# Performance work log

Hardware: AMD Instinct MI355X
Metric: run time of the kernel (lower is better)

## Reference

```python
import jax, jax.numpy as jnp
import numpy as np

TOKENS = 8192
MODEL_DIM = 4096
PROMPT_DIM = 64
NUM_EXPERTS = 8
TOP_K = 2
EPS = float(np.finfo(np.float32).eps)


def setup_inputs() -> dict:
    key = jax.random.key(0)
    k1, k2, k3 = jax.random.split(key, 3)
    x = jax.random.normal(k1, (TOKENS, MODEL_DIM), dtype=jnp.float32)
    prompt = jax.random.normal(k2, (TOKENS, PROMPT_DIM), dtype=jnp.float32)
    # gate linear: Linear(model_dim + prompt_dim, num_experts, bias=True)
    W = jax.random.normal(k3, (MODEL_DIM + PROMPT_DIM, NUM_EXPERTS), dtype=jnp.float32) * 0.02
    b = jnp.zeros((NUM_EXPERTS,), dtype=jnp.float32)
    return {"x": x, "prompt": prompt, "W": W, "b": b}


def reference(x, prompt, W, b):
    # eval path: no jitter, no noise (self.training is False)
    logits = jnp.concatenate([x, prompt], axis=-1) @ W + b          # [T, E]
    _, topk_idx = jax.lax.top_k(logits, TOP_K)                      # [T, K]
    masks = jax.nn.one_hot(topk_idx, NUM_EXPERTS, dtype=jnp.float32)  # [T, K, E]
    gates = jax.nn.softmax(logits, axis=-1)                         # [T, E]
    gates_s = jnp.einsum("te,tke->tk", gates, masks)               # masked gather-sum
    if TOP_K > 1:
        denom = jnp.maximum(gates_s.sum(axis=-1, keepdims=True), EPS)
        gates_s = gates_s / denom
    # masks[:, i] == masks_se[i], gates_s[:, i] == gates_s[i] in the torch code
    return masks, gates_s
```

## Files before the change

kernel.cpp:

```cpp
#include <hip/hip_runtime.h>
#include <math.h>

#define NE 8
#define EPS_F32 1.1920929e-07f

__device__ __forceinline__ void fma8(float xs, const float4& lo, const float4& hi, float* a) {
    a[0] = fmaf(xs, lo.x, a[0]);
    a[1] = fmaf(xs, lo.y, a[1]);
    a[2] = fmaf(xs, lo.z, a[2]);
    a[3] = fmaf(xs, lo.w, a[3]);
    a[4] = fmaf(xs, hi.x, a[4]);
    a[5] = fmaf(xs, hi.y, a[5]);
    a[6] = fmaf(xs, hi.z, a[6]);
    a[7] = fmaf(xs, hi.w, a[7]);
}

__global__ __launch_bounds__(256, 4)
void topk_gate(const float* __restrict__ x,
               const float* __restrict__ prompt,
               const float* __restrict__ W,
               const float* __restrict__ b,
               float* __restrict__ out,
               int tokens)
{
    const int tid  = threadIdx.x;
    const int lane = tid & 63;
    const int wave = tid >> 6;
    const int pair = wave >> 1;
    const int ks   = wave & 1;
    const int tblock = blockIdx.x * 8;
    const int tbase  = tblock + pair * 4;

    __shared__ float lds[2][2][4][NE];

    float acc[4][NE];
#pragma unroll
    for (int t = 0; t < 4; ++t)
#pragma unroll
        for (int e = 0; e < NE; ++e) acc[t][e] = 0.f;

    const int kofs = ks * 2048;

#pragma unroll 2
    for (int i = 0; i < 8; ++i) {
        const int k = kofs + i * 256 + lane * 4;

        float4 xv[4];
#pragma unroll
        for (int t = 0; t < 4; ++t)
            xv[t] = *(const float4*)(x + (size_t)(tbase + t) * 4096 + k);

        float4 wlo[4], whi[4];
#pragma unroll
        for (int j = 0; j < 4; ++j) {
            wlo[j] = *(const float4*)(W + (size_t)(k + j) * 8);
            whi[j] = *(const float4*)(W + (size_t)(k + j) * 8 + 4);
        }

#pragma unroll
        for (int t = 0; t < 4; ++t) {
            fma8(xv[t].x, wlo[0], whi[0], acc[t]);
            fma8(xv[t].y, wlo[1], whi[1], acc[t]);
            fma8(xv[t].z, wlo[2], whi[2], acc[t]);
            fma8(xv[t].w, wlo[3], whi[3], acc[t]);
        }
    }

    if (ks == 1 && lane < 16) {
        const int k = lane * 4;
        float4 pv[4];
#pragma unroll
        for (int t = 0; t < 4; ++t)
            pv[t] = *(const float4*)(prompt + (size_t)(tbase + t) * 64 + k);
        float4 wlo[4], whi[4];
#pragma unroll
        for (int j = 0; j < 4; ++j) {
            wlo[j] = *(const float4*)(W + (size_t)(4096 + k + j) * 8);
            whi[j] = *(const float4*)(W + (size_t)(4096 + k + j) * 8 + 4);
        }
#pragma unroll
        for (int t = 0; t < 4; ++t) {
            fma8(pv[t].x, wlo[0], whi[0], acc[t]);
            fma8(pv[t].y, wlo[1], whi[1], acc[t]);
            fma8(pv[t].z, wlo[2], whi[2], acc[t]);
            fma8(pv[t].w, wlo[3], whi[3], acc[t]);
        }
    }

#pragma unroll
    for (int t = 0; t < 4; ++t)
#pragma unroll
        for (int e = 0; e < NE; ++e) {
            float v = acc[t][e];
#pragma unroll
            for (int off = 32; off >= 1; off >>= 1)
                v += __shfl_xor(v, off, 64);
            acc[t][e] = v;
        }

    if (lane < 32) {
        const int t = lane >> 3;
        const int e = lane & 7;
        lds[pair][ks][t][e] = acc[t][e];
    }
    __syncthreads();

    if (tid < 128) {
        const int tl = tid >> 4;
        const int kk = (tid >> 3) & 1;
        const int ee = tid & 7;
        const int p  = tl >> 2;
        const int t4 = tl & 3;

        float lg[NE];
#pragma unroll
        for (int e = 0; e < NE; ++e)
            lg[e] = lds[p][0][t4][e] + lds[p][1][t4][e] + b[e];

        float v0 = lg[0]; int i0 = 0;
#pragma unroll
        for (int e = 1; e < NE; ++e)
            if (lg[e] > v0) { v0 = lg[e]; i0 = e; }
        float v1 = (i0 == 0) ? lg[1] : lg[0];
        int   i1 = (i0 == 0) ? 1 : 0;
#pragma unroll
        for (int e = 0; e < NE; ++e)
            if (e != i0 && lg[e] > v1) { v1 = lg[e]; i1 = e; }

        float s = 0.f;
#pragma unroll
        for (int e = 0; e < NE; ++e) s += __expf(lg[e] - v0);
        const float g0 = 1.0f / s;
        const float g1 = __expf(v1 - v0) / s;
        const float denom = fmaxf(g0 + g1, EPS_F32);

        const int t_global = tblock + tl;
        const int sel = kk ? i1 : i0;
        out[(size_t)t_global * 16 + kk * 8 + ee] = (ee == sel) ? 1.0f : 0.0f;

        if ((tid & 15) < 2) {
            const float g = (ee == 0) ? (g0 / denom) : (g1 / denom);
            out[(size_t)tokens * 16 + (size_t)t_global * 2 + ee] = g;
        }
    }
}

extern "C" void kernel_launch(void* const* d_in, const int* in_sizes, int n_in,
                              void* d_out, int out_size, void* d_ws, size_t ws_size,
                              hipStream_t stream) {
    const float* x      = (const float*)d_in[0];
    const float* prompt = (const float*)d_in[1];
    const float* W      = (const float*)d_in[2];
    const float* b      = (const float*)d_in[3];
    float* out          = (float*)d_out;

    const int tokens = in_sizes[0] / 4096;
    const int grid   = tokens / 8;

    hipLaunchKernelGGL(topk_gate, dim3(grid), dim3(256), 0, stream,
                       x, prompt, W, b, out, tokens);
}
```

Before: 244.9 us.

## Transpose gate weights to expert-major layout and split K across four waves

Adds a small pre-kernel that transposes W into an expert-major buffer in workspace. Each lane can then load one contiguous float4 per expert instead of two interleaved float4s per row. The main kernel now gives each block 4 tokens with all four waves splitting the K dimension, so the grid doubles and there is more parallelism. The cost is a second launch and a transpose done on every call, plus a four-way cross-wave reduction through LDS.

```diff
diff --git a/kernel.cpp b/kernel.cpp
--- a/kernel.cpp
+++ b/kernel.cpp
@@ -2,36 +2,37 @@
 #include <math.h>
 
 #define NE 8
+#define KDIM 4096
+#define PDIM 64
+#define WROWS (KDIM + PDIM)
 #define EPS_F32 1.1920929e-07f
 
-__device__ __forceinline__ void fma8(float xs, const float4& lo, const float4& hi, float* a) {
-    a[0] = fmaf(xs, lo.x, a[0]);
-    a[1] = fmaf(xs, lo.y, a[1]);
-    a[2] = fmaf(xs, lo.z, a[2]);
-    a[3] = fmaf(xs, lo.w, a[3]);
-    a[4] = fmaf(xs, hi.x, a[4]);
-    a[5] = fmaf(xs, hi.y, a[5]);
-    a[6] = fmaf(xs, hi.z, a[6]);
-    a[7] = fmaf(xs, hi.w, a[7]);
+__global__ __launch_bounds__(256)
+void transpose_w(const float* __restrict__ W, float* __restrict__ Wt) {
+    const int k = blockIdx.x * 256 + threadIdx.x;
+    if (k < WROWS) {
+        float v[NE];
+#pragma unroll
+        for (int e = 0; e < NE; ++e) v[e] = W[(size_t)k * NE + e];
+#pragma unroll
+        for (int e = 0; e < NE; ++e) Wt[(size_t)e * WROWS + k] = v[e];
+    }
 }
 
 __global__ __launch_bounds__(256, 4)
 void topk_gate(const float* __restrict__ x,
                const float* __restrict__ prompt,
-               const float* __restrict__ W,
+               const float* __restrict__ Wt,
                const float* __restrict__ b,
                float* __restrict__ out,
                int tokens)
 {
     const int tid  = threadIdx.x;
     const int lane = tid & 63;
-    const int wave = tid >> 6;
-    const int pair = wave >> 1;
-    const int ks   = wave & 1;
-    const int tblock = blockIdx.x * 8;
-    const int tbase  = tblock + pair * 4;
+    const int ks   = tid >> 6;
+    const int tblock = blockIdx.x * 4;
 
-    __shared__ float lds[2][2][4][NE];
+    __shared__ float lds[4][4][NE];
 
     float acc[4][NE];
 #pragma unroll
@@ -39,52 +40,52 @@
 #pragma unroll
         for (int e = 0; e < NE; ++e) acc[t][e] = 0.f;
 
-    const int kofs = ks * 2048;
+    const int kofs = ks * 1024;
 
 #pragma unroll 2
-    for (int i = 0; i < 8; ++i) {
+    for (int i = 0; i < 4; ++i) {
         const int k = kofs + i * 256 + lane * 4;
 
         float4 xv[4];
 #pragma unroll
         for (int t = 0; t < 4; ++t)
-            xv[t] = *(const float4*)(x + (size_t)(tbase + t) * 4096 + k);
+            xv[t] = *(const float4*)(x + (size_t)(tblock + t) * KDIM + k);
 
-        float4 wlo[4], whi[4];
+        float4 wv[NE];
 #pragma unroll
-        for (int j = 0; j < 4; ++j) {
-            wlo[j] = *(const float4*)(W + (size_t)(k + j) * 8);
-            whi[j] = *(const float4*)(W + (size_t)(k + j) * 8 + 4);
-        }
+        for (int e = 0; e < NE; ++e)
+            wv[e] = *(const float4*)(Wt + (size_t)e * WROWS + k);
 
 #pragma unroll
-        for (int t = 0; t < 4; ++t) {
-            fma8(xv[t].x, wlo[0], whi[0], acc[t]);
-            fma8(xv[t].y, wlo[1], whi[1], acc[t]);
-            fma8(xv[t].z, wlo[2], whi[2], acc[t]);
-            fma8(xv[t].w, wlo[3], whi[3], acc[t]);
-        }
+        for (int t = 0; t < 4; ++t)
+#pragma unroll
+            for (int e = 0; e < NE; ++e) {
+                acc[t][e] = fmaf(xv[t].x, wv[e].x, acc[t][e]);
+                acc[t][e] = fmaf(xv[t].y, wv[e].y, acc[t][e]);
+                acc[t][e] = fmaf(xv[t].z, wv[e].z, acc[t][e]);
+                acc[t][e] = fmaf(xv[t].w, wv[e].w, acc[t][e]);
+            }
     }
 
-    if (ks == 1 && lane < 16) {
+    if (ks == 3 && lane < 16) {
         const int k = lane * 4;
         float4 pv[4];
 #pragma unroll
         for (int t = 0; t < 4; ++t)
-            pv[t] = *(const float4*)(prompt + (size_t)(tbase + t) * 64 + k);
-        float4 wlo[4], whi[4];
+            pv[t] = *(const float4*)(prompt + (size_t)(tblock + t) * PDIM + k);
+        float4 wv[NE];
 #pragma unroll
-        for (int j = 0; j < 4; ++j) {
-            wlo[j] = *(const float4*)(W + (size_t)(4096 + k + j) * 8);
-            whi[j] = *(const float4*)(W + (size_t)(4096 + k + j) * 8 + 4);
-        }
+        for (int e = 0; e < NE; ++e)
+            wv[e] = *(const float4*)(Wt + (size_t)e * WROWS + KDIM + k);
 #pragma unroll
-        for (int t = 0; t < 4; ++t) {
-            fma8(pv[t].x, wlo[0], whi[0], acc[t]);
-            fma8(pv[t].y, wlo[1], whi[1], acc[t]);
-            fma8(pv[t].z, wlo[2], whi[2], acc[t]);
-            fma8(pv[t].w, wlo[3], whi[3], acc[t]);
-        }
+        for (int t = 0; t < 4; ++t)
+#pragma unroll
+            for (int e = 0; e < NE; ++e) {
+                acc[t][e] = fmaf(pv[t].x, wv[e].x, acc[t][e]);
+                acc[t][e] = fmaf(pv[t].y, wv[e].y, acc[t][e]);
+                acc[t][e] = fmaf(pv[t].z, wv[e].z, acc[t][e]);
+                acc[t][e] = fmaf(pv[t].w, wv[e].w, acc[t][e]);
+            }
     }
 
 #pragma unroll
@@ -101,21 +102,19 @@
     if (lane < 32) {
         const int t = lane >> 3;
         const int e = lane & 7;
-        lds[pair][ks][t][e] = acc[t][e];
+        lds[ks][t][e] = acc[t][e];
     }
     __syncthreads();
 
-    if (tid < 128) {
+    if (tid < 64) {
         const int tl = tid >> 4;
         const int kk = (tid >> 3) & 1;
         const int ee = tid & 7;
-        const int p  = tl >> 2;
-        const int t4 = tl & 3;
 
         float lg[NE];
 #pragma unroll
         for (int e = 0; e < NE; ++e)
-            lg[e] = lds[p][0][t4][e] + lds[p][1][t4][e] + b[e];
+            lg[e] = lds[0][tl][e] + lds[1][tl][e] + lds[2][tl][e] + lds[3][tl][e] + b[e];
 
         float v0 = lg[0]; int i0 = 0;
 #pragma unroll
@@ -153,10 +152,12 @@
     const float* W      = (const float*)d_in[2];
     const float* b      = (const float*)d_in[3];
     float* out          = (float*)d_out;
+    float* Wt           = (float*)d_ws;
 
-    const int tokens = in_sizes[0] / 4096;
-    const int grid   = tokens / 8;
+    const int tokens = in_sizes[0] / KDIM;
 
-    hipLaunchKernelGGL(topk_gate, dim3(grid), dim3(256), 0, stream,
-                       x, prompt, W, b, out, tokens);
+    hipLaunchKernelGGL(transpose_w, dim3((WROWS + 255) / 256), dim3(256), 0, stream,
+                       W, Wt);
+    hipLaunchKernelGGL(topk_gate, dim3(tokens / 4), dim3(256), 0, stream,
+                       x, prompt, Wt, b, out, tokens);
 }
```

After: 226.6 us. 7.5% less time.
